# Optimization experiments

Hardware: AMD Instinct MI355X
Metric: run time of the kernel (lower is better)

## Reference

```python
import jax, jax.numpy as jnp
import numpy as np

WS = 16      # window_size
HEADS = 8    # num_heads


def setup_inputs() -> dict:
    key = jax.random.key(0)
    ks = jax.random.split(key, 3)
    B, C, H, W = 16, 512, 64, 64
    x = jax.random.normal(ks[0], (B, C, H, W), dtype=jnp.float32)
    in_proj_w = jax.random.normal(ks[1], (3 * C, C), dtype=jnp.float32) * 0.02
    in_proj_b = jnp.zeros((3 * C,), dtype=jnp.float32)
    out_w = jax.random.normal(ks[2], (C, C), dtype=jnp.float32) * 0.02
    out_b = jnp.zeros((C,), dtype=jnp.float32)
    return {"x": x, "in_proj_w": in_proj_w, "in_proj_b": in_proj_b,
            "out_w": out_w, "out_b": out_b}


def reference(x, in_proj_w, in_proj_b, out_w, out_b):
    B, C, H, W = x.shape
    pad_h = (-H) % WS
    pad_w = (-W) % WS
    x = jnp.pad(x, ((0, 0), (0, 0), (0, pad_h), (0, pad_w)))
    Hp, Wp = x.shape[2], x.shape[3]
    nH, nW = Hp // WS, Wp // WS
    # window partition: (B,C,Hp,Wp) -> (B*nH*nW, WS*WS, C)
    xw = x.reshape(B, C, nH, WS, nW, WS)
    xw = xw.transpose(0, 2, 4, 3, 5, 1).reshape(B * nH * nW, WS * WS, C)
    # torch MHA default batch_first=False: dim0 = seq (L = B*nH*nW), dim1 = batch (N = WS*WS)
    L, N, _ = xw.shape
    d = C // HEADS
    qkv = xw @ in_proj_w.T + in_proj_b            # (L, N, 3C)
    q, k, v = jnp.split(qkv, 3, axis=-1)
    q = q.reshape(L, N, HEADS, d) * (d ** -0.5)
    k = k.reshape(L, N, HEADS, d)
    v = v.reshape(L, N, HEADS, d)
    scores = jnp.einsum('lnhd,mnhd->nhlm', q, k)  # (N, H, L, L)
    attn = jax.nn.softmax(scores, axis=-1)
    o = jnp.einsum('nhlm,mnhd->lnhd', attn, v).reshape(L, N, C)
    o = o @ out_w.T + out_b                       # (L, N, C)
    # window reverse: -> (B, C, Hp, Wp)
    o = o.reshape(B, nH, nW, WS, WS, C).transpose(0, 5, 1, 3, 2, 4)
    o = o.reshape(B, C, Hp, Wp)
    return o[:, :, :H, :W]
```

## Files before the change

### kernel.cpp

```cpp
#include <hip/hip_runtime.h>
#include <stdint.h>
#include <stddef.h>
#include <math.h>


typedef __bf16 bf16;
typedef __attribute__((ext_vector_type(8))) __bf16 bf16x8;
typedef __attribute__((ext_vector_type(4))) __bf16 bf16x4;
typedef __attribute__((ext_vector_type(4))) float f32x4;

#define MFMA16(A, B, C) __builtin_amdgcn_mfma_f32_16x16x32_bf16((A), (B), (C), 0, 0, 0)

__device__ __forceinline__ float fast_exp2(float x) { return exp2f(x); }

__device__ __forceinline__ int aswz(int n, int c) {
  int g = (c >> 3) ^ ((n >> 4) & 7) ^ (n & 7);
  return n * 512 + (g << 3) + (c & 7);
}

__global__ void cvt_fp32_bf16(const float* __restrict__ src, bf16* __restrict__ dst) {
  int i = (blockIdx.x * blockDim.x + threadIdx.x) * 4;
  float4 f = *(const float4*)(src + i);
  bf16x4 r;
  r[0] = (bf16)f.x; r[1] = (bf16)f.y; r[2] = (bf16)f.z; r[3] = (bf16)f.w;
  *(bf16x4*)(dst + i) = r;
}

__global__ void __launch_bounds__(512, 2) gemm_qkv(
    const float* __restrict__ x, const bf16* __restrict__ w1,
    const float* __restrict__ b1,
    bf16* __restrict__ qo, bf16* __restrict__ ko, bf16* __restrict__ vo) {
  extern __shared__ bf16 Al[];
  bf16* Ep = Al + 128 * 512;
  const int tid = threadIdx.x;
  const int bm  = blockIdx.x;
  const int l   = bm >> 1;
  const int n0  = (bm & 1) << 7;
  const int b   = l >> 4, ih = (l >> 2) & 3, iw = l & 3;
  const int h0  = ih * 16 + (n0 >> 4);
  const int w0  = iw * 16;

  for (int j = 0; j < 32; ++j) {
    int f4  = j * 512 + tid;
    int c   = f4 >> 5;
    int qq  = f4 & 31;
    int wsh = qq >> 2;
    int w4  = (qq & 3) << 2;
    float4 xf = *(const float4*)(x + (((b * 512 + c) * 64 + h0 + wsh) * 64 + w0 + w4));
    int nb = wsh * 16 + w4;
    Al[aswz(nb + 0, c)] = (bf16)xf.x;
    Al[aswz(nb + 1, c)] = (bf16)xf.y;
    Al[aswz(nb + 2, c)] = (bf16)xf.z;
    Al[aswz(nb + 3, c)] = (bf16)xf.w;
  }
  __syncthreads();

  const int wave = tid >> 6, lane = tid & 63;
  const int l15 = lane & 15, quad = lane >> 4;
  const int wr = wave >> 2, wc = wave & 3;
  const int R = wr * 64;
  bf16* Epw = Ep + wave * 16 * 72;
  const f32x4 fz = {0.f, 0.f, 0.f, 0.f};

  for (int nc = 0; nc < 6; ++nc) {
    const int t0w = nc * 256 + wc * 64;
    f32x4 acc[4][4];
#pragma unroll
    for (int a = 0; a < 4; ++a)
#pragma unroll
      for (int c2 = 0; c2 < 4; ++c2) acc[a][c2] = fz;

    bf16x8 bfr[4];
#pragma unroll
    for (int ct = 0; ct < 4; ++ct)
      bfr[ct] = *(const bf16x8*)&w1[(size_t)(t0w + ct * 16 + l15) * 512 + quad * 8];
#pragma unroll
    for (int ks = 0; ks < 16; ++ks) {
      bf16x8 bnx[4];
      if (ks < 15) {
#pragma unroll
        for (int ct = 0; ct < 4; ++ct)
          bnx[ct] = *(const bf16x8*)&w1[(size_t)(t0w + ct * 16 + l15) * 512 + (ks + 1) * 32 + quad * 8];
      }
      bf16x8 af[4];
#pragma unroll
      for (int lt = 0; lt < 4; ++lt)
        af[lt] = *(const bf16x8*)&Al[aswz(R + lt * 16 + l15, ks * 32 + quad * 8)];
#pragma unroll
      for (int lt = 0; lt < 4; ++lt)
#pragma unroll
        for (int ct = 0; ct < 4; ++ct)
          acc[lt][ct] = MFMA16(af[lt], bfr[ct], acc[lt][ct]);
#pragma unroll
      for (int ct = 0; ct < 4; ++ct) bfr[ct] = bnx[ct];
    }

    const int which = t0w >> 9;
    const int hh = (t0w & 511) >> 6;
    bf16* dst = (which == 0) ? qo : (which == 1) ? ko : vo;
    const float scale = (which == 0) ? 0.125f : 1.0f;
    float bias[4];
#pragma unroll
    for (int ct = 0; ct < 4; ++ct) bias[ct] = b1[t0w + ct * 16 + l15];

#pragma unroll
    for (int lt = 0; lt < 4; ++lt) {
#pragma unroll
      for (int ct = 0; ct < 4; ++ct)
#pragma unroll
        for (int r = 0; r < 4; ++r)
          Epw[(quad * 4 + r) * 72 + ct * 16 + l15] =
              (bf16)((acc[lt][ct][r] + bias[ct]) * scale);
      const int rr = lane >> 3, ch8 = (lane & 7) * 8;
#pragma unroll
      for (int half = 0; half < 2; ++half) {
        int row = half * 8 + rr;
        bf16x8 vv = *(const bf16x8*)&Epw[row * 72 + ch8];
        int n = n0 + R + lt * 16 + row;
        *(bf16x8*)&dst[((size_t)(n * 8 + hh) * 256 + l) * 64 + ch8] = vv;
      }
    }
  }
}

__global__ void __launch_bounds__(512, 2) attn_win(
    bf16* __restrict__ qio, const bf16* __restrict__ kg, const bf16* __restrict__ vg) {
  extern __shared__ bf16 sm[];
  bf16* Kl = sm;
  bf16* Vt = sm + 256 * 72;
  bf16* Pl = Vt + 64 * 264;
  const int tid = threadIdx.x;
  const int bb = blockIdx.x;
  const int n = bb >> 3, h = bb & 7;
  const size_t base = (size_t)(n * 8 + h) * 16384;
  const bf16* Kg = kg + base;
  const bf16* Vg = vg + base;
  bf16* Qg = qio + base;

  for (int j = 0; j < 4; ++j) {
    int cc = j * 512 + tid;
    int m = cc >> 3, dc = cc & 7;
    bf16x8 t = *(const bf16x8*)(Kg + m * 64 + dc * 8);
    *(bf16x8*)&Kl[m * 72 + dc * 8] = t;
  }
  for (int j = 0; j < 4; ++j) {
    int cc = j * 512 + tid;
    int dc = cc >> 8, m = cc & 255;
    bf16x8 t = *(const bf16x8*)(Vg + m * 64 + dc * 8);
#pragma unroll
    for (int s = 0; s < 8; ++s) Vt[(dc * 8 + s) * 264 + m] = t[s];
  }

  const int wave = tid >> 6, lane = tid & 63;
  const int l15 = lane & 15, quad = lane >> 4;
  const int lb = wave * 32;
  bf16* Pw = Pl + wave * 16 * 264;

  bf16x8 qf[2][2];
#pragma unroll
  for (int lt = 0; lt < 2; ++lt)
#pragma unroll
    for (int ks = 0; ks < 2; ++ks)
      qf[lt][ks] = *(const bf16x8*)(Qg + (lb + lt * 16 + l15) * 64 + ks * 32 + quad * 8);

  __syncthreads();

  const f32x4 fz = {0.f, 0.f, 0.f, 0.f};
  const float LOG2E = 1.44269504088896340736f;
  for (int lt = 0; lt < 2; ++lt) {
    f32x4 s[16];
#pragma unroll
    for (int mt = 0; mt < 16; ++mt) s[mt] = fz;
#pragma unroll
    for (int mt = 0; mt < 16; ++mt)
#pragma unroll
      for (int ks = 0; ks < 2; ++ks) {
        bf16x8 kf = *(const bf16x8*)&Kl[(mt * 16 + l15) * 72 + ks * 32 + quad * 8];
        s[mt] = MFMA16(qf[lt][ks], kf, s[mt]);
      }
    float rmax[4], rsum[4];
#pragma unroll
    for (int r = 0; r < 4; ++r) {
      float mx = s[0][r];
#pragma unroll
      for (int mt = 1; mt < 16; ++mt) mx = fmaxf(mx, s[mt][r]);
#pragma unroll
      for (int xo = 1; xo < 16; xo <<= 1) mx = fmaxf(mx, __shfl_xor(mx, xo, 16));
      rmax[r] = mx;
      rsum[r] = 0.f;
    }
#pragma unroll
    for (int mt = 0; mt < 16; ++mt) {
#pragma unroll
      for (int r = 0; r < 4; ++r) {
        float p = fast_exp2((s[mt][r] - rmax[r]) * LOG2E);
        bf16 pb = (bf16)p;
        rsum[r] += (float)pb;
        Pw[(quad * 4 + r) * 264 + mt * 16 + l15] = pb;
      }
    }
#pragma unroll
    for (int r = 0; r < 4; ++r)
#pragma unroll
      for (int xo = 1; xo < 16; xo <<= 1) rsum[r] += __shfl_xor(rsum[r], xo, 16);

    bf16x8 pf[8];
#pragma unroll
    for (int mk = 0; mk < 8; ++mk)
      pf[mk] = *(const bf16x8*)&Pw[l15 * 264 + mk * 32 + quad * 8];
    f32x4 of[4];
#pragma unroll
    for (int dt = 0; dt < 4; ++dt) of[dt] = fz;
#pragma unroll
    for (int dt = 0; dt < 4; ++dt)
#pragma unroll
      for (int mk = 0; mk < 8; ++mk) {
        bf16x8 vf = *(const bf16x8*)&Vt[(dt * 16 + l15) * 264 + mk * 32 + quad * 8];
        of[dt] = MFMA16(pf[mk], vf, of[dt]);
      }
    float inv[4];
#pragma unroll
    for (int r = 0; r < 4; ++r) inv[r] = 1.0f / rsum[r];

    bf16* Ew = Pw;
#pragma unroll
    for (int dt = 0; dt < 4; ++dt)
#pragma unroll
      for (int r = 0; r < 4; ++r)
        Ew[(quad * 4 + r) * 72 + dt * 16 + l15] = (bf16)(of[dt][r] * inv[r]);
    const int rr = lane >> 3, ch8 = (lane & 7) * 8;
#pragma unroll
    for (int half = 0; half < 2; ++half) {
      int row = half * 8 + rr;
      bf16x8 vv = *(const bf16x8*)&Ew[row * 72 + ch8];
      *(bf16x8*)(Qg + (lb + lt * 16 + row) * 64 + ch8) = vv;
    }
  }
}

__global__ void __launch_bounds__(512, 2) gemm_out(
    const bf16* __restrict__ og, const bf16* __restrict__ w2,
    const float* __restrict__ b2, float* __restrict__ out) {
  extern __shared__ bf16 Al[];
  const int tid = threadIdx.x;
  const int bm = blockIdx.x;
  const int l = bm >> 1;
  const int n0 = (bm & 1) << 7;
  const int b = l >> 4, ih = (l >> 2) & 3, iw = l & 3;

  for (int j = 0; j < 16; ++j) {
    int cc = j * 512 + tid;
    int nl = cc >> 6;
    int ch = cc & 63;
    int hh = ch >> 3, d8 = (ch & 7) * 8;
    bf16x8 t = *(const bf16x8*)(og + ((size_t)((n0 + nl) * 8 + hh) * 256 + l) * 64 + d8);
    *(bf16x8*)&Al[aswz(nl, ch * 8)] = t;
  }
  __syncthreads();

  const int wave = tid >> 6, lane = tid & 63;
  const int l15 = lane & 15, quad = lane >> 4;
  const int wr = wave >> 2, wc = wave & 3;
  const int R = wr * 64;
  const f32x4 fz = {0.f, 0.f, 0.f, 0.f};

  for (int nc = 0; nc < 2; ++nc) {
    const int t0w = nc * 256 + wc * 64;
    f32x4 acc[4][4];
#pragma unroll
    for (int a = 0; a < 4; ++a)
#pragma unroll
      for (int c2 = 0; c2 < 4; ++c2) acc[a][c2] = fz;

    bf16x8 bfr[4];
#pragma unroll
    for (int ct = 0; ct < 4; ++ct)
      bfr[ct] = *(const bf16x8*)&w2[(size_t)(t0w + ct * 16 + l15) * 512 + quad * 8];
#pragma unroll
    for (int ks = 0; ks < 16; ++ks) {
      bf16x8 bnx[4];
      if (ks < 15) {
#pragma unroll
        for (int ct = 0; ct < 4; ++ct)
          bnx[ct] = *(const bf16x8*)&w2[(size_t)(t0w + ct * 16 + l15) * 512 + (ks + 1) * 32 + quad * 8];
      }
      bf16x8 af[4];
#pragma unroll
      for (int lt = 0; lt < 4; ++lt)
        af[lt] = *(const bf16x8*)&Al[aswz(R + lt * 16 + l15, ks * 32 + quad * 8)];
#pragma unroll
      for (int lt = 0; lt < 4; ++lt)
#pragma unroll
        for (int ct = 0; ct < 4; ++ct)
          acc[lt][ct] = MFMA16(bfr[ct], af[lt], acc[lt][ct]);
#pragma unroll
      for (int ct = 0; ct < 4; ++ct) bfr[ct] = bnx[ct];
    }

#pragma unroll
    for (int ct = 0; ct < 4; ++ct) {
      float4 bias4 = *(const float4*)&b2[t0w + ct * 16 + quad * 4];
#pragma unroll
      for (int lt = 0; lt < 4; ++lt) {
        const int nbase = n0 + R + lt * 16;
        const int wsh = nbase >> 4;
        size_t rowbase = (((size_t)b * 512) * 64 + (size_t)ih * 16 + wsh) * 64 + iw * 16 + l15;
#pragma unroll
        for (int r = 0; r < 4; ++r) {
          int cout = t0w + ct * 16 + quad * 4 + r;
          out[rowbase + (size_t)cout * 4096] = acc[lt][ct][r] + ((const float*)&bias4)[r];
        }
      }
    }
  }
}

extern "C" void kernel_launch(void* const* d_in, const int* in_sizes, int n_in,
                              void* d_out, int out_size, void* d_ws, size_t ws_size,
                              hipStream_t stream) {
  (void)in_sizes; (void)n_in; (void)out_size; (void)ws_size;
  const float* x   = (const float*)d_in[0];
  const float* w1f = (const float*)d_in[1];
  const float* b1  = (const float*)d_in[2];
  const float* w2f = (const float*)d_in[3];
  const float* b2  = (const float*)d_in[4];
  float* out = (float*)d_out;

  char* ws = (char*)d_ws;
  bf16* q   = (bf16*)(ws);
  bf16* k   = (bf16*)(ws + 67108864ull);
  bf16* v   = (bf16*)(ws + 134217728ull);
  bf16* w1b = (bf16*)(ws + 201326592ull);
  bf16* w2b = (bf16*)(ws + 201326592ull + 1572864ull);

  const int LDS_QKV  = (128 * 512 + 8 * 16 * 72) * 2;
  const int LDS_ATTN = (256 * 72 + 64 * 264 + 8 * 16 * 264) * 2;
  const int LDS_OUT  = 128 * 512 * 2;
  hipFuncSetAttribute(reinterpret_cast<const void*>(gemm_qkv),
                      hipFuncAttributeMaxDynamicSharedMemorySize, LDS_QKV);
  hipFuncSetAttribute(reinterpret_cast<const void*>(attn_win),
                      hipFuncAttributeMaxDynamicSharedMemorySize, LDS_ATTN);
  hipFuncSetAttribute(reinterpret_cast<const void*>(gemm_out),
                      hipFuncAttributeMaxDynamicSharedMemorySize, LDS_OUT);

  hipLaunchKernelGGL(cvt_fp32_bf16, dim3(768), dim3(256), 0, stream, w1f, w1b);
  hipLaunchKernelGGL(cvt_fp32_bf16, dim3(256), dim3(256), 0, stream, w2f, w2b);
  hipLaunchKernelGGL(gemm_qkv, dim3(512), dim3(512), LDS_QKV, stream, x, w1b, b1, q, k, v);
  hipLaunchKernelGGL(attn_win, dim3(2048), dim3(512), LDS_ATTN, stream, q, k, v);
  hipLaunchKernelGGL(gemm_out, dim3(512), dim3(512), LDS_OUT, stream, q, w2b, b2, out);
}
```

Measured before the change: 690.1 us.

## Double GEMM workgroups to 1024 threads, transpose MFMA outputs, restructure attention softmax

Both projection GEMMs move to 1024-thread blocks with 16 waves, so each block needs fewer column-chunk iterations over the same staged LDS tile. The QKV epilogue now uses swapped MFMA operands, vectorized bf16x4 LDS writes and two barrier-separated phases so the halves of the block share one scratch buffer. The attention kernel swaps operands so each lane holds a full score row, which reduces the row max/sum to two cross-lane shuffles. It also interleaves the two row tiles in the PV MFMA loop and switches exp2 to the hardware builtin. The risks are higher register pressure under launch_bounds(1024,4) and extra barriers in the QKV epilogue.

```diff
diff --git a/kernel.cpp b/kernel.cpp
--- a/kernel.cpp
+++ b/kernel.cpp
@@ -11,7 +11,13 @@
 
 #define MFMA16(A, B, C) __builtin_amdgcn_mfma_f32_16x16x32_bf16((A), (B), (C), 0, 0, 0)
 
-__device__ __forceinline__ float fast_exp2(float x) { return exp2f(x); }
+__device__ __forceinline__ float fast_exp2(float x) {
+#if __has_builtin(__builtin_amdgcn_exp2f)
+  return __builtin_amdgcn_exp2f(x);
+#else
+  return exp2f(x);
+#endif
+}
 
 __device__ __forceinline__ int aswz(int n, int c) {
   int g = (c >> 3) ^ ((n >> 4) & 7) ^ (n & 7);
@@ -26,7 +32,7 @@
   *(bf16x4*)(dst + i) = r;
 }
 
-__global__ void __launch_bounds__(512, 2) gemm_qkv(
+__global__ void __launch_bounds__(1024, 4) gemm_qkv(
     const float* __restrict__ x, const bf16* __restrict__ w1,
     const float* __restrict__ b1,
     bf16* __restrict__ qo, bf16* __restrict__ ko, bf16* __restrict__ vo) {
@@ -40,8 +46,8 @@
   const int h0  = ih * 16 + (n0 >> 4);
   const int w0  = iw * 16;
 
-  for (int j = 0; j < 32; ++j) {
-    int f4  = j * 512 + tid;
+  for (int j = 0; j < 16; ++j) {
+    int f4  = j * 1024 + tid;
     int c   = f4 >> 5;
     int qq  = f4 & 31;
     int wsh = qq >> 2;
@@ -57,13 +63,12 @@
 
   const int wave = tid >> 6, lane = tid & 63;
   const int l15 = lane & 15, quad = lane >> 4;
-  const int wr = wave >> 2, wc = wave & 3;
+  const int wr = wave >> 3, wc = wave & 7;
   const int R = wr * 64;
-  bf16* Epw = Ep + wave * 16 * 72;
   const f32x4 fz = {0.f, 0.f, 0.f, 0.f};
 
-  for (int nc = 0; nc < 6; ++nc) {
-    const int t0w = nc * 256 + wc * 64;
+  for (int nc = 0; nc < 3; ++nc) {
+    const int t0w = nc * 512 + wc * 64;
     f32x4 acc[4][4];
 #pragma unroll
     for (int a = 0; a < 4; ++a)
@@ -90,34 +95,39 @@
       for (int lt = 0; lt < 4; ++lt)
 #pragma unroll
         for (int ct = 0; ct < 4; ++ct)
-          acc[lt][ct] = MFMA16(af[lt], bfr[ct], acc[lt][ct]);
+          acc[lt][ct] = MFMA16(bfr[ct], af[lt], acc[lt][ct]);
 #pragma unroll
       for (int ct = 0; ct < 4; ++ct) bfr[ct] = bnx[ct];
     }
 
-    const int which = t0w >> 9;
-    const int hh = (t0w & 511) >> 6;
-    bf16* dst = (which == 0) ? qo : (which == 1) ? ko : vo;
-    const float scale = (which == 0) ? 0.125f : 1.0f;
-    float bias[4];
-#pragma unroll
-    for (int ct = 0; ct < 4; ++ct) bias[ct] = b1[t0w + ct * 16 + l15];
-
-#pragma unroll
-    for (int lt = 0; lt < 4; ++lt) {
-#pragma unroll
-      for (int ct = 0; ct < 4; ++ct)
-#pragma unroll
-        for (int r = 0; r < 4; ++r)
-          Epw[(quad * 4 + r) * 72 + ct * 16 + l15] =
-              (bf16)((acc[lt][ct][r] + bias[ct]) * scale);
-      const int rr = lane >> 3, ch8 = (lane & 7) * 8;
-#pragma unroll
-      for (int half = 0; half < 2; ++half) {
-        int row = half * 8 + rr;
-        bf16x8 vv = *(const bf16x8*)&Epw[row * 72 + ch8];
-        int n = n0 + R + lt * 16 + row;
-        *(bf16x8*)&dst[((size_t)(n * 8 + hh) * 256 + l) * 64 + ch8] = vv;
+    bf16* dst = (nc == 0) ? qo : (nc == 1) ? ko : vo;
+    const float scale = (nc == 0) ? 0.125f : 1.0f;
+
+#pragma unroll
+    for (int phase = 0; phase < 2; ++phase) {
+      __syncthreads();
+      if (wr == phase) {
+        bf16* Epw = Ep + wc * 16 * 72;
+#pragma unroll
+        for (int lt = 0; lt < 4; ++lt) {
+#pragma unroll
+          for (int ct = 0; ct < 4; ++ct) {
+            float4 bias4 = *(const float4*)&b1[t0w + ct * 16 + quad * 4];
+            bf16x4 pk;
+#pragma unroll
+            for (int r = 0; r < 4; ++r)
+              pk[r] = (bf16)((acc[lt][ct][r] + ((const float*)&bias4)[r]) * scale);
+            *(bf16x4*)&Epw[l15 * 72 + ct * 16 + quad * 4] = pk;
+          }
+          const int rr = lane >> 3, ch8 = (lane & 7) * 8;
+#pragma unroll
+          for (int hf = 0; hf < 2; ++hf) {
+            int row = hf * 8 + rr;
+            bf16x8 vv = *(const bf16x8*)&Epw[row * 72 + ch8];
+            int n = n0 + R + lt * 16 + row;
+            *(bf16x8*)&dst[((size_t)(n * 8 + wc) * 256 + l) * 64 + ch8] = vv;
+          }
+        }
       }
     }
   }
@@ -167,6 +177,10 @@
 
   const f32x4 fz = {0.f, 0.f, 0.f, 0.f};
   const float LOG2E = 1.44269504088896340736f;
+  float inv[2];
+  bf16x8 pf[2][8];
+
+#pragma unroll
   for (int lt = 0; lt < 2; ++lt) {
     f32x4 s[16];
 #pragma unroll
@@ -176,69 +190,70 @@
 #pragma unroll
       for (int ks = 0; ks < 2; ++ks) {
         bf16x8 kf = *(const bf16x8*)&Kl[(mt * 16 + l15) * 72 + ks * 32 + quad * 8];
-        s[mt] = MFMA16(qf[lt][ks], kf, s[mt]);
-      }
-    float rmax[4], rsum[4];
-#pragma unroll
-    for (int r = 0; r < 4; ++r) {
-      float mx = s[0][r];
-#pragma unroll
-      for (int mt = 1; mt < 16; ++mt) mx = fmaxf(mx, s[mt][r]);
-#pragma unroll
-      for (int xo = 1; xo < 16; xo <<= 1) mx = fmaxf(mx, __shfl_xor(mx, xo, 16));
-      rmax[r] = mx;
-      rsum[r] = 0.f;
-    }
+        s[mt] = MFMA16(kf, qf[lt][ks], s[mt]);
+      }
+    float mx = s[0][0];
+#pragma unroll
+    for (int mt = 0; mt < 16; ++mt)
+#pragma unroll
+      for (int r = 0; r < 4; ++r) mx = fmaxf(mx, s[mt][r]);
+    mx = fmaxf(mx, __shfl_xor(mx, 16));
+    mx = fmaxf(mx, __shfl_xor(mx, 32));
+    float sum = 0.f;
 #pragma unroll
     for (int mt = 0; mt < 16; ++mt) {
+      bf16x4 pk;
 #pragma unroll
       for (int r = 0; r < 4; ++r) {
-        float p = fast_exp2((s[mt][r] - rmax[r]) * LOG2E);
+        float p = fast_exp2((s[mt][r] - mx) * LOG2E);
         bf16 pb = (bf16)p;
-        rsum[r] += (float)pb;
-        Pw[(quad * 4 + r) * 264 + mt * 16 + l15] = pb;
-      }
-    }
-#pragma unroll
-    for (int r = 0; r < 4; ++r)
-#pragma unroll
-      for (int xo = 1; xo < 16; xo <<= 1) rsum[r] += __shfl_xor(rsum[r], xo, 16);
-
-    bf16x8 pf[8];
+        sum += (float)pb;
+        pk[r] = pb;
+      }
+      *(bf16x4*)&Pw[l15 * 264 + mt * 16 + quad * 4] = pk;
+    }
+    sum += __shfl_xor(sum, 16);
+    sum += __shfl_xor(sum, 32);
+    inv[lt] = 1.0f / sum;
 #pragma unroll
     for (int mk = 0; mk < 8; ++mk)
-      pf[mk] = *(const bf16x8*)&Pw[l15 * 264 + mk * 32 + quad * 8];
-    f32x4 of[4];
-#pragma unroll
-    for (int dt = 0; dt < 4; ++dt) of[dt] = fz;
-#pragma unroll
-    for (int dt = 0; dt < 4; ++dt)
-#pragma unroll
-      for (int mk = 0; mk < 8; ++mk) {
-        bf16x8 vf = *(const bf16x8*)&Vt[(dt * 16 + l15) * 264 + mk * 32 + quad * 8];
-        of[dt] = MFMA16(pf[mk], vf, of[dt]);
-      }
-    float inv[4];
-#pragma unroll
-    for (int r = 0; r < 4; ++r) inv[r] = 1.0f / rsum[r];
-
-    bf16* Ew = Pw;
-#pragma unroll
-    for (int dt = 0; dt < 4; ++dt)
-#pragma unroll
-      for (int r = 0; r < 4; ++r)
-        Ew[(quad * 4 + r) * 72 + dt * 16 + l15] = (bf16)(of[dt][r] * inv[r]);
+      pf[lt][mk] = *(const bf16x8*)&Pw[l15 * 264 + mk * 32 + quad * 8];
+  }
+
+  f32x4 of[2][4];
+#pragma unroll
+  for (int lt = 0; lt < 2; ++lt)
+#pragma unroll
+    for (int dt = 0; dt < 4; ++dt) of[lt][dt] = fz;
+#pragma unroll
+  for (int dt = 0; dt < 4; ++dt)
+#pragma unroll
+    for (int mk = 0; mk < 8; ++mk) {
+      bf16x8 vf = *(const bf16x8*)&Vt[(dt * 16 + l15) * 264 + mk * 32 + quad * 8];
+      of[0][dt] = MFMA16(vf, pf[0][mk], of[0][dt]);
+      of[1][dt] = MFMA16(vf, pf[1][mk], of[1][dt]);
+    }
+
+#pragma unroll
+  for (int lt = 0; lt < 2; ++lt) {
+#pragma unroll
+    for (int dt = 0; dt < 4; ++dt) {
+      bf16x4 pk;
+#pragma unroll
+      for (int r = 0; r < 4; ++r) pk[r] = (bf16)(of[lt][dt][r] * inv[lt]);
+      *(bf16x4*)&Pw[l15 * 264 + dt * 16 + quad * 4] = pk;
+    }
     const int rr = lane >> 3, ch8 = (lane & 7) * 8;
 #pragma unroll
-    for (int half = 0; half < 2; ++half) {
-      int row = half * 8 + rr;
-      bf16x8 vv = *(const bf16x8*)&Ew[row * 72 + ch8];
+    for (int hf = 0; hf < 2; ++hf) {
+      int row = hf * 8 + rr;
+      bf16x8 vv = *(const bf16x8*)&Pw[row * 264 + ch8];
       *(bf16x8*)(Qg + (lb + lt * 16 + row) * 64 + ch8) = vv;
     }
   }
 }
 
-__global__ void __launch_bounds__(512, 2) gemm_out(
+__global__ void __launch_bounds__(1024, 4) gemm_out(
     const bf16* __restrict__ og, const bf16* __restrict__ w2,
     const float* __restrict__ b2, float* __restrict__ out) {
   extern __shared__ bf16 Al[];
@@ -248,8 +263,8 @@
   const int n0 = (bm & 1) << 7;
   const int b = l >> 4, ih = (l >> 2) & 3, iw = l & 3;
 
-  for (int j = 0; j < 16; ++j) {
-    int cc = j * 512 + tid;
+  for (int j = 0; j < 8; ++j) {
+    int cc = j * 1024 + tid;
     int nl = cc >> 6;
     int ch = cc & 63;
     int hh = ch >> 3, d8 = (ch & 7) * 8;
@@ -260,56 +275,54 @@
 
   const int wave = tid >> 6, lane = tid & 63;
   const int l15 = lane & 15, quad = lane >> 4;
-  const int wr = wave >> 2, wc = wave & 3;
+  const int wr = wave >> 3, wc = wave & 7;
   const int R = wr * 64;
+  const int t0w = wc * 64;
   const f32x4 fz = {0.f, 0.f, 0.f, 0.f};
 
-  for (int nc = 0; nc < 2; ++nc) {
-    const int t0w = nc * 256 + wc * 64;
-    f32x4 acc[4][4];
-#pragma unroll
-    for (int a = 0; a < 4; ++a)
-#pragma unroll
-      for (int c2 = 0; c2 < 4; ++c2) acc[a][c2] = fz;
-
-    bf16x8 bfr[4];
-#pragma unroll
-    for (int ct = 0; ct < 4; ++ct)
-      bfr[ct] = *(const bf16x8*)&w2[(size_t)(t0w + ct * 16 + l15) * 512 + quad * 8];
-#pragma unroll
-    for (int ks = 0; ks < 16; ++ks) {
-      bf16x8 bnx[4];
-      if (ks < 15) {
-#pragma unroll
-        for (int ct = 0; ct < 4; ++ct)
-          bnx[ct] = *(const bf16x8*)&w2[(size_t)(t0w + ct * 16 + l15) * 512 + (ks + 1) * 32 + quad * 8];
-      }
-      bf16x8 af[4];
-#pragma unroll
-      for (int lt = 0; lt < 4; ++lt)
-        af[lt] = *(const bf16x8*)&Al[aswz(R + lt * 16 + l15, ks * 32 + quad * 8)];
-#pragma unroll
-      for (int lt = 0; lt < 4; ++lt)
-#pragma unroll
-        for (int ct = 0; ct < 4; ++ct)
-          acc[lt][ct] = MFMA16(bfr[ct], af[lt], acc[lt][ct]);
-#pragma unroll
-      for (int ct = 0; ct < 4; ++ct) bfr[ct] = bnx[ct];
-    }
-
-#pragma unroll
-    for (int ct = 0; ct < 4; ++ct) {
-      float4 bias4 = *(const float4*)&b2[t0w + ct * 16 + quad * 4];
-#pragma unroll
-      for (int lt = 0; lt < 4; ++lt) {
-        const int nbase = n0 + R + lt * 16;
-        const int wsh = nbase >> 4;
-        size_t rowbase = (((size_t)b * 512) * 64 + (size_t)ih * 16 + wsh) * 64 + iw * 16 + l15;
-#pragma unroll
-        for (int r = 0; r < 4; ++r) {
-          int cout = t0w + ct * 16 + quad * 4 + r;
-          out[rowbase + (size_t)cout * 4096] = acc[lt][ct][r] + ((const float*)&bias4)[r];
-        }
+  f32x4 acc[4][4];
+#pragma unroll
+  for (int a = 0; a < 4; ++a)
+#pragma unroll
+    for (int c2 = 0; c2 < 4; ++c2) acc[a][c2] = fz;
+
+  bf16x8 bfr[4];
+#pragma unroll
+  for (int ct = 0; ct < 4; ++ct)
+    bfr[ct] = *(const bf16x8*)&w2[(size_t)(t0w + ct * 16 + l15) * 512 + quad * 8];
+#pragma unroll
+  for (int ks = 0; ks < 16; ++ks) {
+    bf16x8 bnx[4];
+    if (ks < 15) {
+#pragma unroll
+      for (int ct = 0; ct < 4; ++ct)
+        bnx[ct] = *(const bf16x8*)&w2[(size_t)(t0w + ct * 16 + l15) * 512 + (ks + 1) * 32 + quad * 8];
+    }
+    bf16x8 af[4];
+#pragma unroll
+    for (int lt = 0; lt < 4; ++lt)
+      af[lt] = *(const bf16x8*)&Al[aswz(R + lt * 16 + l15, ks * 32 + quad * 8)];
+#pragma unroll
+    for (int lt = 0; lt < 4; ++lt)
+#pragma unroll
+      for (int ct = 0; ct < 4; ++ct)
+        acc[lt][ct] = MFMA16(bfr[ct], af[lt], acc[lt][ct]);
+#pragma unroll
+    for (int ct = 0; ct < 4; ++ct) bfr[ct] = bnx[ct];
+  }
+
+#pragma unroll
+  for (int ct = 0; ct < 4; ++ct) {
+    float4 bias4 = *(const float4*)&b2[t0w + ct * 16 + quad * 4];
+#pragma unroll
+    for (int lt = 0; lt < 4; ++lt) {
+      const int nbase = n0 + R + lt * 16;
+      const int wsh = nbase >> 4;
+      size_t rowbase = (((size_t)b * 512) * 64 + (size_t)ih * 16 + wsh) * 64 + iw * 16 + l15;
+#pragma unroll
+      for (int r = 0; r < 4; ++r) {
+        int cout = t0w + ct * 16 + quad * 4 + r;
+        out[rowbase + (size_t)cout * 4096] = acc[lt][ct][r] + ((const float*)&bias4)[r];
       }
     }
   }
@@ -345,7 +358,7 @@
 
   hipLaunchKernelGGL(cvt_fp32_bf16, dim3(768), dim3(256), 0, stream, w1f, w1b);
   hipLaunchKernelGGL(cvt_fp32_bf16, dim3(256), dim3(256), 0, stream, w2f, w2b);
-  hipLaunchKernelGGL(gemm_qkv, dim3(512), dim3(512), LDS_QKV, stream, x, w1b, b1, q, k, v);
+  hipLaunchKernelGGL(gemm_qkv, dim3(512), dim3(1024), LDS_QKV, stream, x, w1b, b1, q, k, v);
   hipLaunchKernelGGL(attn_win, dim3(2048), dim3(512), LDS_ATTN, stream, q, k, v);
-  hipLaunchKernelGGL(gemm_out, dim3(512), dim3(512), LDS_OUT, stream, q, w2b, b2, out);
-}
+  hipLaunchKernelGGL(gemm_out, dim3(512), dim3(1024), LDS_OUT, stream, q, w2b, b2, out);
+}
```

Measured after the change: 814.6 us. 1.18x slower.
